# Optimization experiments

Hardware: AMD Instinct MI355X
Metric: run time of the kernel (lower is better)

The kernel has to match this reference:

```python
import jax, jax.numpy as jnp
import numpy as np

LN_EPS = 1e-5

def _ln(x, g, b):
    mu = jnp.mean(x, axis=-1, keepdims=True)
    var = jnp.mean((x - mu) ** 2, axis=-1, keepdims=True)
    return (x - mu) * jax.lax.rsqrt(var + LN_EPS) * g + b

def _gelu(x):
    return jax.nn.gelu(x, approximate=False)

def _time_embed(t, dim):
    # standard sinusoidal embedding on scalar times t: (B,) -> (B, dim)
    half = dim // 2
    freqs = jnp.exp(-jnp.log(10000.0) * jnp.arange(half, dtype=jnp.float32) / max(half - 1, 1))
    ang = t[:, None] * freqs[None, :]
    return jnp.concatenate([jnp.sin(ang), jnp.cos(ang)], axis=-1)

def setup_inputs() -> dict:
    key = jax.random.key(0)
    B, D, C, H, M = 1024, 128, 256, 512, 64
    ks = jax.random.split(key, 24)
    w = lambda k, shp: jax.random.normal(k, shp, dtype=jnp.float32) * 0.02
    inp = {
        "noise": jax.random.normal(ks[0], (B, D), dtype=jnp.float32),
        "context": jax.random.normal(ks[1], (B, C), dtype=jnp.float32),
        "support_memory": jax.random.normal(ks[2], (B, M, D), dtype=jnp.float32),
        "num_steps": 4,
        # memory adapter: LayerNorm(D) + Linear(D->H)
        "mem_ln_g": jnp.ones((D,), jnp.float32), "mem_ln_b": jnp.zeros((D,), jnp.float32),
        "Wa": w(ks[3], (D, H)), "ba": jnp.zeros((H,), jnp.float32),
        # attention projections H->H
        "Wq": w(ks[4], (H, H)), "bq": jnp.zeros((H,), jnp.float32),
        "Wk": w(ks[5], (H, H)), "bk": jnp.zeros((H,), jnp.float32),
        "Wv": w(ks[6], (H, H)), "bv": jnp.zeros((H,), jnp.float32),
        "Wo": w(ks[7], (H, H)), "bo": jnp.zeros((H,), jnp.float32),
        # particle proj: LN(D) + Linear(D->H) + GELU + Linear(H->H)
        "pp_ln_g": jnp.ones((D,), jnp.float32), "pp_ln_b": jnp.zeros((D,), jnp.float32),
        "Wp1": w(ks[8], (D, H)), "bp1": jnp.zeros((H,), jnp.float32),
        "Wp2": w(ks[9], (H, H)), "bp2": jnp.zeros((H,), jnp.float32),
        # context proj C->H
        "Wc": w(ks[10], (C, H)), "bc": jnp.zeros((H,), jnp.float32),
        # time proj H->H (on sinusoidal embedding of dim H)
        "Wt": w(ks[11], (H, H)), "bt": jnp.zeros((H,), jnp.float32),
        # fusion head: LN(4H) + Linear(4H->H) + GELU + Linear(H->D)
        "f_ln_g": jnp.ones((4 * H,), jnp.float32), "f_ln_b": jnp.zeros((4 * H,), jnp.float32),
        "Wf1": w(ks[12], (4 * H, H)), "bf1": jnp.zeros((H,), jnp.float32),
        "Wf2": w(ks[13], (H, D)), "bf2": jnp.zeros((D,), jnp.float32),
    }
    return inp

def reference(noise, context, support_memory, num_steps,
              mem_ln_g, mem_ln_b, Wa, ba,
              Wq, bq, Wk, bk, Wv, bv, Wo, bo,
              pp_ln_g, pp_ln_b, Wp1, bp1, Wp2, bp2,
              Wc, bc, Wt, bt,
              f_ln_g, f_ln_b, Wf1, bf1, Wf2, bf2):
    B, D = noise.shape
    H = Wq.shape[0]
    heads = 4
    dh = H // heads
    scale = dh ** -0.5

    # encode support memory once (solver-invariant), like encode_memory()
    enc = _ln(support_memory, mem_ln_g, mem_ln_b) @ Wa + ba            # (B, M, H)
    M = enc.shape[1]
    k_mem = (enc @ Wk + bk).reshape(B, M, heads, dh)                    # (B, M, h, dh)
    v_mem = (enc @ Wv + bv).reshape(B, M, heads, dh)
    ctx_h = context @ Wc + bc                                           # (B, H)

    def velocity(y, t):
        te = _time_embed(t, H) @ Wt + bt                                # (B, H)
        h = _gelu(_ln(y, pp_ln_g, pp_ln_b) @ Wp1 + bp1) @ Wp2 + bp2      # (B, H)
        q = (h @ Wq + bq).reshape(B, heads, dh)
        logits = jnp.einsum('bhd,bmhd->bhm', q, k_mem) * scale
        attn = jax.nn.softmax(logits, axis=-1)
        summ = jnp.einsum('bhm,bmhd->bhd', attn, v_mem).reshape(B, H)
        m = summ @ Wo + bo                                              # (B, H)
        z = jnp.concatenate([h, m, ctx_h, te], axis=-1)                 # (B, 4H)
        return _gelu(_ln(z, f_ln_g, f_ln_b) @ Wf1 + bf1) @ Wf2 + bf2     # (B, D)

    dt = 1.0 / float(num_steps)
    t0s = jnp.arange(num_steps, dtype=jnp.float32) * dt

    def heun_step(y, t0):
        tb0 = jnp.full((B,), t0, dtype=y.dtype)
        k1 = velocity(y, tb0)
        k2 = velocity(y + dt * k1, tb0 + dt)
        return y + 0.5 * dt * (k1 + k2), None

    y_final, _ = jax.lax.scan(heun_step, noise, t0s)
    return y_final
```

## Files before the change

kernel.cpp:

```cpp
#include <hip/hip_runtime.h>
#include <hip/hip_bf16.h>
#include <cstdint>
#include <cstddef>

#define LN_EPS 1e-5f

typedef __attribute__((ext_vector_type(8))) short short8;
typedef __attribute__((ext_vector_type(4))) float f32x4;

__device__ __forceinline__ float gelu_exact(float x) {
  return 0.5f * x * (1.0f + erff(x * 0.70710678118654752440f));
}
__device__ __forceinline__ float bflo(unsigned int x) {
  union { unsigned int i; float f; } v; v.i = x << 16; return v.f;
}
__device__ __forceinline__ float bfhi(unsigned int x) {
  union { unsigned int i; float f; } v; v.i = x & 0xffff0000u; return v.f;
}
__device__ __forceinline__ float bf2f(short s) {
  union { unsigned int i; float f; } v; v.i = ((unsigned int)(unsigned short)s) << 16; return v.f;
}
__device__ __forceinline__ short bf16s(float f) {
  __hip_bfloat16 h = __float2bfloat16(f);
  return *reinterpret_cast<short*>(&h);
}

__global__ __launch_bounds__(256) void ln_bf16_k(const float* __restrict__ X,
                                                 const float* __restrict__ KIN, float a,
                                                 const float* __restrict__ g,
                                                 const float* __restrict__ bb,
                                                 __hip_bfloat16* __restrict__ out, int rows) {
  int row = blockIdx.x * 4 + (threadIdx.x >> 6);
  if (row >= rows) return;
  int l = threadIdx.x & 63;
  size_t base = (size_t)row * 128;
  float x0 = X[base + l], x1 = X[base + l + 64];
  if (KIN) { x0 += a * KIN[base + l]; x1 += a * KIN[base + l + 64]; }
  float s = x0 + x1;
#pragma unroll
  for (int o = 32; o > 0; o >>= 1) s += __shfl_xor(s, o);
  float mu = s * (1.0f / 128.0f);
  float d0 = x0 - mu, d1 = x1 - mu;
  float v = d0 * d0 + d1 * d1;
#pragma unroll
  for (int o = 32; o > 0; o >>= 1) v += __shfl_xor(v, o);
  float rstd = rsqrtf(v * (1.0f / 128.0f) + LN_EPS);
  out[base + l] = __float2bfloat16(d0 * rstd * g[l] + bb[l]);
  out[base + l + 64] = __float2bfloat16(d1 * rstd * g[l + 64] + bb[l + 64]);
}

template <int BN, bool GELU_OUT, bool OUT_BF16>
__global__ __launch_bounds__(256) void gemm_mfma_k(
    const short* __restrict__ A, const short* __restrict__ WT,
    const float* __restrict__ bias, void* __restrict__ Cout,
    int K, int lda, int ldw, int ldc, float alpha,
    int hsA, int hsB, long hsC) {
  constexpr int NFRAG = BN / 16;
  constexpr int NB = (BN / 32) < 1 ? 1 : (BN / 32);
  __shared__ __align__(16) short As[2][64][72];
  __shared__ __align__(16) short Bs[2][BN][72];
  A += (size_t)blockIdx.z * hsA;
  WT += (size_t)blockIdx.z * hsB;
  const size_t cOff = (size_t)blockIdx.z * (size_t)hsC;
  const int tid = threadIdx.x;
  const int w = tid >> 6, l = tid & 63;
  const int row0 = blockIdx.y * 64, col0 = blockIdx.x * BN;
  f32x4 acc[NFRAG];
#pragma unroll
  for (int i = 0; i < NFRAG; ++i) acc[i] = (f32x4){0.f, 0.f, 0.f, 0.f};

  const int nt = K >> 6;
  short8 aR0, aR1;
  short8 bR[NB];
  auto loadA = [&](int t) {
    int k0 = t * 64;
    int c1 = tid + 256;
    aR0 = *(const short8*)(A + (size_t)(row0 + (tid >> 3)) * lda + k0 + (tid & 7) * 8);
    aR1 = *(const short8*)(A + (size_t)(row0 + (c1 >> 3)) * lda + k0 + (c1 & 7) * 8);
  };
  auto loadB = [&](int t) {
    int k0 = t * 64;
#pragma unroll
    for (int i = 0; i < NB; ++i) {
      int c = tid + i * 256;
      bR[i] = *(const short8*)(WT + (size_t)(col0 + (c >> 3)) * ldw + k0 + (c & 7) * 8);
    }
  };
  auto storeT = [&](int buf) {
    int c1 = tid + 256;
    *(short8*)&As[buf][tid >> 3][(tid & 7) * 8] = aR0;
    *(short8*)&As[buf][c1 >> 3][(c1 & 7) * 8] = aR1;
#pragma unroll
    for (int i = 0; i < NB; ++i) {
      int c = tid + i * 256;
      *(short8*)&Bs[buf][c >> 3][(c & 7) * 8] = bR[i];
    }
  };

  loadA(0);
  loadB(0);
  for (int t = 0; t < nt; ++t) {
    int buf = t & 1;
    storeT(buf);
    __syncthreads();
    if (t + 1 < nt) { loadA(t + 1); loadB(t + 1); }
    short8 af0 = *(const short8*)&As[buf][w * 16 + (l & 15)][(l >> 4) * 8];
    short8 af1 = *(const short8*)&As[buf][w * 16 + (l & 15)][(l >> 4) * 8 + 32];
#pragma unroll
    for (int nc = 0; nc < NFRAG; ++nc) {
      short8 bf0 = *(const short8*)&Bs[buf][nc * 16 + (l & 15)][(l >> 4) * 8];
      acc[nc] = __builtin_amdgcn_mfma_f32_16x16x32_bf16(af0, bf0, acc[nc], 0, 0, 0);
      short8 bf1 = *(const short8*)&Bs[buf][nc * 16 + (l & 15)][(l >> 4) * 8 + 32];
      acc[nc] = __builtin_amdgcn_mfma_f32_16x16x32_bf16(af1, bf1, acc[nc], 0, 0, 0);
    }
    __syncthreads();
  }
  const int cr = (l >> 4) * 4;
  const int cc = l & 15;
#pragma unroll
  for (int nc = 0; nc < NFRAG; ++nc) {
    int gc = col0 + nc * 16 + cc;
    float bv = bias ? bias[gc] : 0.0f;
#pragma unroll
    for (int r = 0; r < 4; ++r) {
      int gr = row0 + w * 16 + cr + r;
      float v = acc[nc][r] * alpha + bv;
      if (GELU_OUT) v = gelu_exact(v);
      if (OUT_BF16)
        ((__hip_bfloat16*)Cout)[cOff + (size_t)gr * ldc + gc] = __float2bfloat16(v);
      else
        ((float*)Cout)[cOff + (size_t)gr * ldc + gc] = v;
    }
  }
}

__global__ __launch_bounds__(256) void gemm_heun_k(
    const short* __restrict__ A, const short* __restrict__ WT,
    const float* __restrict__ bias, const float* __restrict__ yin,
    const float* __restrict__ kaux, float c0, float* __restrict__ outY) {
  __shared__ __align__(16) short As[2][64][72];
  __shared__ __align__(16) short Bs[2][32][72];
  const int tid = threadIdx.x;
  const int w = tid >> 6, l = tid & 63;
  const int row0 = blockIdx.y * 64, col0 = blockIdx.x * 32;
  f32x4 acc[2];
  acc[0] = (f32x4){0.f, 0.f, 0.f, 0.f};
  acc[1] = (f32x4){0.f, 0.f, 0.f, 0.f};
  short8 aR0, aR1, bR;
  auto loadA = [&](int t) {
    int k0 = t * 64;
    int c1 = tid + 256;
    aR0 = *(const short8*)(A + (size_t)(row0 + (tid >> 3)) * 512 + k0 + (tid & 7) * 8);
    aR1 = *(const short8*)(A + (size_t)(row0 + (c1 >> 3)) * 512 + k0 + (c1 & 7) * 8);
  };
  auto loadB = [&](int t) {
    int k0 = t * 64;
    bR = *(const short8*)(WT + (size_t)(col0 + (tid >> 3)) * 512 + k0 + (tid & 7) * 8);
  };
  auto storeT = [&](int buf) {
    int c1 = tid + 256;
    *(short8*)&As[buf][tid >> 3][(tid & 7) * 8] = aR0;
    *(short8*)&As[buf][c1 >> 3][(c1 & 7) * 8] = aR1;
    *(short8*)&Bs[buf][tid >> 3][(tid & 7) * 8] = bR;
  };
  loadA(0);
  loadB(0);
  for (int t = 0; t < 8; ++t) {
    int buf = t & 1;
    storeT(buf);
    __syncthreads();
    if (t + 1 < 8) { loadA(t + 1); loadB(t + 1); }
    short8 af0 = *(const short8*)&As[buf][w * 16 + (l & 15)][(l >> 4) * 8];
    short8 af1 = *(const short8*)&As[buf][w * 16 + (l & 15)][(l >> 4) * 8 + 32];
#pragma unroll
    for (int nc = 0; nc < 2; ++nc) {
      short8 bf0 = *(const short8*)&Bs[buf][nc * 16 + (l & 15)][(l >> 4) * 8];
      acc[nc] = __builtin_amdgcn_mfma_f32_16x16x32_bf16(af0, bf0, acc[nc], 0, 0, 0);
      short8 bf1 = *(const short8*)&Bs[buf][nc * 16 + (l & 15)][(l >> 4) * 8 + 32];
      acc[nc] = __builtin_amdgcn_mfma_f32_16x16x32_bf16(af1, bf1, acc[nc], 0, 0, 0);
    }
    __syncthreads();
  }
  const int cr = (l >> 4) * 4, cc = l & 15;
#pragma unroll
  for (int nc = 0; nc < 2; ++nc) {
    int gc = col0 + nc * 16 + cc;
    float bv = bias[gc];
#pragma unroll
    for (int r = 0; r < 4; ++r) {
      int gr = row0 + w * 16 + cr + r;
      float v = acc[nc][r] + bv;
      size_t idx = (size_t)gr * 128 + gc;
      outY[idx] = yin[idx] + c0 * (kaux[idx] + v);
    }
  }
}

struct TCBatch { const float* src[5]; short* dst[5]; };
__global__ __launch_bounds__(256) void transpose_cast_batch_k(TCBatch p) {
  const float* W = p.src[blockIdx.z];
  short* WT = p.dst[blockIdx.z];
  __shared__ float tile[64][65];
  int n0 = blockIdx.x * 64, k0 = blockIdx.y * 64;
#pragma unroll
  for (int i = 0; i < 16; ++i) {
    int e = threadIdx.x + i * 256;
    int r = e >> 6, c = e & 63;
    tile[r][c] = W[(size_t)(k0 + r) * 512 + n0 + c];
  }
  __syncthreads();
#pragma unroll
  for (int i = 0; i < 16; ++i) {
    int e = threadIdx.x + i * 256;
    int r = e >> 6, c = e & 63;
    WT[(size_t)(n0 + r) * 512 + k0 + c] = bf16s(tile[c][r]);
  }
}

__global__ __launch_bounds__(256) void transpose_cast_k(const float* __restrict__ W,
                                                        short* __restrict__ WT,
                                                        int K, int N) {
  __shared__ float tile[64][65];
  int n0 = blockIdx.x * 64, k0 = blockIdx.y * 64;
#pragma unroll
  for (int i = 0; i < 16; ++i) {
    int e = threadIdx.x + i * 256;
    int r = e >> 6, c = e & 63;
    tile[r][c] = W[(size_t)(k0 + r) * N + n0 + c];
  }
  __syncthreads();
#pragma unroll
  for (int i = 0; i < 16; ++i) {
    int e = threadIdx.x + i * 256;
    int r = e >> 6, c = e & 63;
    WT[(size_t)(n0 + r) * K + k0 + c] = bf16s(tile[c][r]);
  }
}

__global__ void cast_bf16_k(const float* __restrict__ src, short* __restrict__ dst, int n) {
  int i = blockIdx.x * blockDim.x + threadIdx.x;
  if (i < n) dst[i] = bf16s(src[i]);
}

__global__ __launch_bounds__(256) void bias_fuse_k(const float* __restrict__ va,
                                                   const float* __restrict__ Wx,
                                                   const float* __restrict__ bx,
                                                   float* __restrict__ out) {
  const int tid = threadIdx.x;
  const int j = blockIdx.x * 32 + (tid >> 3);
  const int kl = tid & 7;
  float s = 0.f;
  for (int k = kl; k < 512; k += 8) s += va[k] * Wx[(size_t)k * 512 + j];
  s += __shfl_xor(s, 1);
  s += __shfl_xor(s, 2);
  s += __shfl_xor(s, 4);
  if (kl == 0) out[j] = s + bx[j];
}

__global__ __launch_bounds__(256) void bqp_k(const float* __restrict__ bhqq,
                                             const short* __restrict__ Wak_bf,
                                             float scale, float* __restrict__ bqp) {
  const int tid = threadIdx.x;
  const int j = blockIdx.x * 32 + (tid >> 3);
  const int h = j >> 7, e = j & 127;
  const int kl = tid & 7;
  float s = 0.f;
  for (int d = kl; d < 128; d += 8)
    s += bhqq[h * 128 + d] * bf2f(Wak_bf[(size_t)e * 512 + h * 128 + d]);
  s += __shfl_xor(s, 1);
  s += __shfl_xor(s, 2);
  s += __shfl_xor(s, 4);
  if (kl == 0) bqp[j] = s * scale;
}

__global__ __launch_bounds__(512) void te_k(const float* __restrict__ Wt,
                                            const float* __restrict__ bt,
                                            float* __restrict__ te) {
  __shared__ float emb[512];
  const int ci = blockIdx.x;
  const float t = 0.25f * (float)((ci >> 1) + (ci & 1));
  const int j = threadIdx.x;
  if (j < 256) {
    float fr = expf(-9.210340371976184f * (float)j * (1.0f / 255.0f));
    float ang = t * fr;
    emb[j] = sinf(ang);
    emb[j + 256] = cosf(ang);
  }
  __syncthreads();
  float s0 = 0.f, s1 = 0.f, s2 = 0.f, s3 = 0.f;
  for (int k = 0; k < 512; k += 4) {
    s0 += emb[k] * Wt[(size_t)k * 512 + j];
    s1 += emb[k + 1] * Wt[(size_t)(k + 1) * 512 + j];
    s2 += emb[k + 2] * Wt[(size_t)(k + 2) * 512 + j];
    s3 += emb[k + 3] * Wt[(size_t)(k + 3) * 512 + j];
  }
  te[(size_t)ci * 512 + j] = bt[j] + ((s0 + s1) + (s2 + s3));
}

__global__ __launch_bounds__(256) void attn_k(const __hip_bfloat16* __restrict__ hq,
                                              const short* __restrict__ lnsm,
                                              __hip_bfloat16* __restrict__ sctx) {
  const int b = blockIdx.x;
  const int tid = threadIdx.x;
  const int w = tid >> 6, l = tid & 63;
  __shared__ __align__(16) short smt[64 * 128];
  __shared__ float qs[512];
  __shared__ float att[4][64];
  {
    unsigned int u = ((const unsigned int*)(hq + (size_t)b * 1024 + 512))[tid];
    qs[2 * tid] = bflo(u);
    qs[2 * tid + 1] = bfhi(u);
  }
  {
    const int m = tid >> 2;
    const short* src = lnsm + ((size_t)b * 64 + m) * 128;
#pragma unroll
    for (int j = 0; j < 4; ++j) {
      int c = (tid & 3) + 4 * j;
      short8 v = *(const short8*)(src + c * 8);
      *(short8*)&smt[m * 128 + ((c ^ (m & 7)) * 8)] = v;
    }
  }
  __syncthreads();
  const float* qh = qs + w * 128;
  float acc = 0.f;
#pragma unroll
  for (int i = 0; i < 16; ++i) {
    uint4 u = *(const uint4*)&smt[l * 128 + ((i ^ (l & 7)) * 8)];
    const int d = i * 8;
    acc += bflo(u.x) * qh[d + 0] + bfhi(u.x) * qh[d + 1] +
           bflo(u.y) * qh[d + 2] + bfhi(u.y) * qh[d + 3] +
           bflo(u.z) * qh[d + 4] + bfhi(u.z) * qh[d + 5] +
           bflo(u.w) * qh[d + 6] + bfhi(u.w) * qh[d + 7];
  }
  float mx = acc;
#pragma unroll
  for (int o = 32; o > 0; o >>= 1) mx = fmaxf(mx, __shfl_xor(mx, o));
  float e = expf(acc - mx);
  float se = e;
#pragma unroll
  for (int o = 32; o > 0; o >>= 1) se += __shfl_xor(se, o);
  att[w][l] = e / se;
  const int cb = l >> 2, doff = 2 * (l & 3);
  float a0 = 0.f, a1 = 0.f;
#pragma unroll 8
  for (int m = 0; m < 64; ++m) {
    float am = att[w][m];
    unsigned int u = *(const unsigned int*)&smt[m * 128 + ((cb ^ (m & 7)) * 8) + doff];
    a0 += am * bflo(u);
    a1 += am * bfhi(u);
  }
  unsigned int pr = ((unsigned int)(unsigned short)bf16s(a1) << 16) |
                    (unsigned int)(unsigned short)bf16s(a0);
  ((unsigned int*)(sctx + (size_t)b * 512 + w * 128))[l] = pr;
}

__global__ __launch_bounds__(512) void zln_k(const __hip_bfloat16* __restrict__ hq,
                                             const __hip_bfloat16* __restrict__ mo,
                                             const __hip_bfloat16* __restrict__ ctxh,
                                             const float* __restrict__ te_row,
                                             const float* __restrict__ g,
                                             const float* __restrict__ bb,
                                             __hip_bfloat16* __restrict__ zout) {
  const int b = blockIdx.x;
  const int tid = threadIdx.x;
  float v0 = __bfloat162float(hq[(size_t)b * 1024 + tid]);
  float v1 = __bfloat162float(mo[(size_t)b * 512 + tid]);
  float v2 = __bfloat162float(ctxh[(size_t)b * 512 + tid]);
  float v3 = te_row[tid];
  __shared__ float red[8];
  float s = v0 + v1 + v2 + v3;
#pragma unroll
  for (int o = 32; o > 0; o >>= 1) s += __shfl_xor(s, o);
  if ((tid & 63) == 0) red[tid >> 6] = s;
  __syncthreads();
  s = red[0] + red[1] + red[2] + red[3] + red[4] + red[5] + red[6] + red[7];
  float mu = s * (1.0f / 2048.0f);
  float d0 = v0 - mu, d1 = v1 - mu, d2 = v2 - mu, d3 = v3 - mu;
  float vv = d0 * d0 + d1 * d1 + d2 * d2 + d3 * d3;
  __syncthreads();
#pragma unroll
  for (int o = 32; o > 0; o >>= 1) vv += __shfl_xor(vv, o);
  if ((tid & 63) == 0) red[tid >> 6] = vv;
  __syncthreads();
  vv = red[0] + red[1] + red[2] + red[3] + red[4] + red[5] + red[6] + red[7];
  float rstd = rsqrtf(vv * (1.0f / 2048.0f) + LN_EPS);
  zout[(size_t)b * 2048 + tid] = __float2bfloat16(d0 * rstd * g[tid] + bb[tid]);
  zout[(size_t)b * 2048 + 512 + tid] = __float2bfloat16(d1 * rstd * g[512 + tid] + bb[512 + tid]);
  zout[(size_t)b * 2048 + 1024 + tid] = __float2bfloat16(d2 * rstd * g[1024 + tid] + bb[1024 + tid]);
  zout[(size_t)b * 2048 + 1536 + tid] = __float2bfloat16(d3 * rstd * g[1536 + tid] + bb[1536 + tid]);
}

extern "C" void kernel_launch(void* const* d_in, const int* in_sizes, int n_in,
                              void* d_out, int out_size, void* d_ws, size_t ws_size,
                              hipStream_t stream) {
  (void)in_sizes; (void)n_in; (void)out_size; (void)ws_size;
  const int B = 1024, Mm = 64;
  const int BMrows = B * Mm;
  const float ATTN_SCALE = 0.08838834764831845f;
  const size_t SL = (size_t)512 * 512;

  const float* noise = (const float*)d_in[0];
  const float* context = (const float*)d_in[1];
  const float* sm = (const float*)d_in[2];
  const float* mem_ln_g = (const float*)d_in[4];
  const float* mem_ln_b = (const float*)d_in[5];
  const float* Wa = (const float*)d_in[6];
  const float* ba = (const float*)d_in[7];
  const float* Wq = (const float*)d_in[8];
  const float* bq = (const float*)d_in[9];
  const float* Wk = (const float*)d_in[10];
  const float* bk = (const float*)d_in[11];
  (void)bk;
  const float* Wv = (const float*)d_in[12];
  const float* bv = (const float*)d_in[13];
  const float* Wo = (const float*)d_in[14];
  const float* bo = (const float*)d_in[15];
  const float* pp_ln_g = (const float*)d_in[16];
  const float* pp_ln_b = (const float*)d_in[17];
  const float* Wp1 = (const float*)d_in[18];
  const float* bp1 = (const float*)d_in[19];
  const float* Wp2 = (const float*)d_in[20];
  const float* bp2 = (const float*)d_in[21];
  const float* Wc = (const float*)d_in[22];
  const float* bc = (const float*)d_in[23];
  const float* Wt = (const float*)d_in[24];
  const float* bt = (const float*)d_in[25];
  const float* f_ln_g = (const float*)d_in[26];
  const float* f_ln_b = (const float*)d_in[27];
  const float* Wf1 = (const float*)d_in[28];
  const float* bf1 = (const float*)d_in[29];
  const float* Wf2 = (const float*)d_in[30];
  const float* bf2 = (const float*)d_in[31];
  float* out = (float*)d_out;

  char* wsb = (char*)d_ws;
  size_t off = 0;
  auto alloc = [&](size_t bytes) -> void* {
    off = (off + 255) & ~(size_t)255;
    void* p = wsb + off;
    off += bytes;
    return p;
  };
  short* lnsm = (short*)alloc((size_t)BMrows * 128 * 2);
  short* T512 = (short*)alloc(4 * SL * 2);
  short* WkT = T512;
  short* WvT = T512 + SL;
  short* WqT = T512 + 2 * SL;
  short* WoT = T512 + 3 * SL;
  short* Wp1T = (short*)alloc((size_t)512 * 128 * 2);
  short* WhqT = (short*)alloc((size_t)1024 * 512 * 2);
  short* WfoldT = (short*)alloc(SL * 2);
  short* WcT = (short*)alloc((size_t)512 * 256 * 2);
  short* Wf1T = (short*)alloc((size_t)512 * 2048 * 2);
  short* Wf2T = (short*)alloc((size_t)128 * 512 * 2);
  short* WaB = (short*)alloc((size_t)128 * 512 * 2);
  short* Wp2B = (short*)alloc(SL * 2);
  short* WakavB = (short*)alloc(2 * (size_t)128 * 512 * 2);
  short* Wak_bf = WakavB;
  short* Wav_bf = WakavB + (size_t)128 * 512;
  short* Wp2q_bf = (short*)alloc(SL * 2);
  float* bhq = (float*)alloc(1024 * 4);
  float* bofold = (float*)alloc(512 * 4);
  float* bhqq = (float*)alloc(512 * 4);
  float* bav = (float*)alloc(512 * 4);
  float* te_table = (float*)alloc(8 * 512 * 4);
  short* ctxh = (short*)alloc((size_t)B * 512 * 2);
  float* k1 = (float*)alloc((size_t)B * 128 * 4);
  float* ybuf = (float*)alloc((size_t)B * 128 * 4);
  short* ctxb = (short*)alloc((size_t)B * 256 * 2);
  short* yln = (short*)alloc((size_t)B * 128 * 2);
  short* hmid = (short*)alloc((size_t)B * 512 * 2);
  short* hqbuf = (short*)alloc((size_t)B * 1024 * 2);
  short* sctx = (short*)alloc((size_t)B * 512 * 2);
  short* mobuf = (short*)alloc((size_t)B * 512 * 2);
  short* zbuf = (short*)alloc((size_t)B * 2048 * 2);
  short* fmid = (short*)alloc((size_t)B * 512 * 2);

  ln_bf16_k<<<BMrows / 4, 256, 0, stream>>>(sm, nullptr, 0.f, mem_ln_g, mem_ln_b,
                                            (__hip_bfloat16*)lnsm, BMrows);
  cast_bf16_k<<<(128 * 512 + 255) / 256, 256, 0, stream>>>(Wa, WaB, 128 * 512);
  cast_bf16_k<<<(512 * 512 + 255) / 256, 256, 0, stream>>>(Wp2, Wp2B, 512 * 512);
  cast_bf16_k<<<(B * 256 + 255) / 256, 256, 0, stream>>>(context, ctxb, B * 256);
  {
    TCBatch p;
    p.src[0] = Wk; p.src[1] = Wv; p.src[2] = Wq; p.src[3] = Wo; p.src[4] = Wp2;
    p.dst[0] = WkT; p.dst[1] = WvT; p.dst[2] = WqT; p.dst[3] = WoT; p.dst[4] = WhqT;
    transpose_cast_batch_k<<<dim3(8, 8, 5), 256, 0, stream>>>(p);
  }
  transpose_cast_k<<<dim3(8, 2), 256, 0, stream>>>(Wp1, Wp1T, 128, 512);
  transpose_cast_k<<<dim3(8, 4), 256, 0, stream>>>(Wc, WcT, 256, 512);
  transpose_cast_k<<<dim3(8, 32), 256, 0, stream>>>(Wf1, Wf1T, 2048, 512);
  transpose_cast_k<<<dim3(2, 8), 256, 0, stream>>>(Wf2, Wf2T, 512, 128);
  gemm_mfma_k<64, false, true><<<dim3(8, 2, 2), 256, 0, stream>>>(
      WaB, WkT, nullptr, WakavB, 512, 512, 512, 512, 1.f, 0, (int)SL, 128 * 512);
  gemm_mfma_k<64, false, true><<<dim3(8, 8), 256, 0, stream>>>(
      Wp2B, WqT, nullptr, Wp2q_bf, 512, 512, 512, 512, 1.f, 0, 0, 0);
  gemm_mfma_k<64, false, true><<<dim3(8, 2, 4), 256, 0, stream>>>(
      Wak_bf, Wp2q_bf, nullptr, WhqT + SL, 128, 512, 512, 512, ATTN_SCALE,
      128, 128, 128 * 512);
  gemm_mfma_k<64, false, true><<<dim3(2, 8, 4), 256, 0, stream>>>(
      WoT, Wav_bf, nullptr, WfoldT, 128, 512, 512, 512, 1.f, 128, 128, 128);
  bias_fuse_k<<<16, 256, 0, stream>>>(bp2, Wq, bq, bhqq);
  bqp_k<<<16, 256, 0, stream>>>(bhqq, Wak_bf, ATTN_SCALE, bhq + 512);
  hipMemcpyAsync(bhq, bp2, 512 * 4, hipMemcpyDeviceToDevice, stream);
  bias_fuse_k<<<16, 256, 0, stream>>>(ba, Wv, bv, bav);
  bias_fuse_k<<<16, 256, 0, stream>>>(bav, Wo, bo, bofold);
  gemm_mfma_k<64, false, true><<<dim3(8, 16), 256, 0, stream>>>(
      ctxb, WcT, bc, ctxh, 256, 256, 256, 512, 1.f, 0, 0, 0);
  te_k<<<8, 512, 0, stream>>>(Wt, bt, te_table);

  const float dt = 0.25f;
  auto chain = [&](const float* ycur, const float* kin, float a, int tidx) {
    ln_bf16_k<<<B / 4, 256, 0, stream>>>(ycur, kin, a, pp_ln_g, pp_ln_b,
                                         (__hip_bfloat16*)yln, B);
    gemm_mfma_k<32, true, true><<<dim3(16, 16), 256, 0, stream>>>(
        yln, Wp1T, bp1, hmid, 128, 128, 128, 512, 1.f, 0, 0, 0);
    gemm_mfma_k<64, false, true><<<dim3(16, 16), 256, 0, stream>>>(
        hmid, WhqT, bhq, hqbuf, 512, 512, 512, 1024, 1.f, 0, 0, 0);
    attn_k<<<B, 256, 0, stream>>>((const __hip_bfloat16*)hqbuf, lnsm,
                                  (__hip_bfloat16*)sctx);
    gemm_mfma_k<32, false, true><<<dim3(16, 16), 256, 0, stream>>>(
        sctx, WfoldT, bofold, mobuf, 512, 512, 512, 512, 1.f, 0, 0, 0);
    zln_k<<<B, 512, 0, stream>>>((const __hip_bfloat16*)hqbuf, (const __hip_bfloat16*)mobuf,
                                 (const __hip_bfloat16*)ctxh, te_table + (size_t)tidx * 512,
                                 f_ln_g, f_ln_b, (__hip_bfloat16*)zbuf);
    gemm_mfma_k<32, true, true><<<dim3(16, 16), 256, 0, stream>>>(
        zbuf, Wf1T, bf1, fmid, 2048, 2048, 2048, 512, 1.f, 0, 0, 0);
  };

  const float* ycur = noise;
  for (int s = 0; s < 4; ++s) {
    chain(ycur, nullptr, 0.f, 2 * s);
    gemm_mfma_k<32, false, false><<<dim3(4, 16), 256, 0, stream>>>(
        fmid, Wf2T, bf2, k1, 512, 512, 512, 128, 1.f, 0, 0, 0);
    chain(ycur, k1, dt, 2 * s + 1);
    float* ynext = (s == 3) ? out : ybuf;
    gemm_heun_k<<<dim3(4, 16), 256, 0, stream>>>(
        fmid, Wf2T, bf2, ycur, k1, 0.5f * dt, ynext);
    ycur = ybuf;
  }
}
```

Measured before the change: 596.9 us.

## Replace LDS-tiled GEMMs in the ODE loop with single-wave register-direct MFMA kernels

```diff
diff --git a/kernel.cpp b/kernel.cpp
--- a/kernel.cpp
+++ b/kernel.cpp
@@ -47,6 +47,56 @@
   float rstd = rsqrtf(v * (1.0f / 128.0f) + LN_EPS);
   out[base + l] = __float2bfloat16(d0 * rstd * g[l] + bb[l]);
   out[base + l + 64] = __float2bfloat16(d1 * rstd * g[l + 64] + bb[l + 64]);
+}
+
+template <int K, int COLS, int EPI, bool GELU_OUT, bool OUT_BF16>
+__global__ __launch_bounds__(64) void gemm_wave_k(
+    const short* __restrict__ A, const short* __restrict__ WT,
+    const float* __restrict__ bias, void* __restrict__ Cout,
+    int lda, int ldw, int ldc,
+    const float* __restrict__ yin, const float* __restrict__ kaux, float c0) {
+  constexpr int F = COLS / 16;
+  const int l = threadIdx.x;
+  const int row0 = blockIdx.y * 16, col0 = blockIdx.x * COLS;
+  const int rl = l & 15, k8 = (l >> 4) * 8;
+  const short* pA = A + (size_t)(row0 + rl) * lda + k8;
+  const short* pB[F];
+#pragma unroll
+  for (int f = 0; f < F; ++f)
+    pB[f] = WT + (size_t)(col0 + f * 16 + rl) * ldw + k8;
+  f32x4 acc[F];
+#pragma unroll
+  for (int f = 0; f < F; ++f) acc[f] = (f32x4){0.f, 0.f, 0.f, 0.f};
+#pragma unroll
+  for (int k0 = 0; k0 < K; k0 += 32) {
+    short8 a = *(const short8*)(pA + k0);
+    short8 b[F];
+#pragma unroll
+    for (int f = 0; f < F; ++f) b[f] = *(const short8*)(pB[f] + k0);
+#pragma unroll
+    for (int f = 0; f < F; ++f)
+      acc[f] = __builtin_amdgcn_mfma_f32_16x16x32_bf16(a, b[f], acc[f], 0, 0, 0);
+  }
+  const int cr = (l >> 4) * 4, cc = l & 15;
+#pragma unroll
+  for (int f = 0; f < F; ++f) {
+    int gc = col0 + f * 16 + cc;
+    float bv = bias ? bias[gc] : 0.0f;
+#pragma unroll
+    for (int r = 0; r < 4; ++r) {
+      int gr = row0 + cr + r;
+      float v = acc[f][r] + bv;
+      if (GELU_OUT) v = gelu_exact(v);
+      size_t idx = (size_t)gr * ldc + gc;
+      if (EPI == 2) {
+        ((float*)Cout)[idx] = yin[idx] + c0 * (kaux[idx] + v);
+      } else if (OUT_BF16) {
+        ((__hip_bfloat16*)Cout)[idx] = __float2bfloat16(v);
+      } else {
+        ((float*)Cout)[idx] = v;
+      }
+    }
+  }
 }
 
 template <int BN, bool GELU_OUT, bool OUT_BF16>
@@ -130,68 +180,6 @@
         ((__hip_bfloat16*)Cout)[cOff + (size_t)gr * ldc + gc] = __float2bfloat16(v);
       else
         ((float*)Cout)[cOff + (size_t)gr * ldc + gc] = v;
-    }
-  }
-}
-
-__global__ __launch_bounds__(256) void gemm_heun_k(
-    const short* __restrict__ A, const short* __restrict__ WT,
-    const float* __restrict__ bias, const float* __restrict__ yin,
-    const float* __restrict__ kaux, float c0, float* __restrict__ outY) {
-  __shared__ __align__(16) short As[2][64][72];
-  __shared__ __align__(16) short Bs[2][32][72];
-  const int tid = threadIdx.x;
-  const int w = tid >> 6, l = tid & 63;
-  const int row0 = blockIdx.y * 64, col0 = blockIdx.x * 32;
-  f32x4 acc[2];
-  acc[0] = (f32x4){0.f, 0.f, 0.f, 0.f};
-  acc[1] = (f32x4){0.f, 0.f, 0.f, 0.f};
-  short8 aR0, aR1, bR;
-  auto loadA = [&](int t) {
-    int k0 = t * 64;
-    int c1 = tid + 256;
-    aR0 = *(const short8*)(A + (size_t)(row0 + (tid >> 3)) * 512 + k0 + (tid & 7) * 8);
-    aR1 = *(const short8*)(A + (size_t)(row0 + (c1 >> 3)) * 512 + k0 + (c1 & 7) * 8);
-  };
-  auto loadB = [&](int t) {
-    int k0 = t * 64;
-    bR = *(const short8*)(WT + (size_t)(col0 + (tid >> 3)) * 512 + k0 + (tid & 7) * 8);
-  };
-  auto storeT = [&](int buf) {
-    int c1 = tid + 256;
-    *(short8*)&As[buf][tid >> 3][(tid & 7) * 8] = aR0;
-    *(short8*)&As[buf][c1 >> 3][(c1 & 7) * 8] = aR1;
-    *(short8*)&Bs[buf][tid >> 3][(tid & 7) * 8] = bR;
-  };
-  loadA(0);
-  loadB(0);
-  for (int t = 0; t < 8; ++t) {
-    int buf = t & 1;
-    storeT(buf);
-    __syncthreads();
-    if (t + 1 < 8) { loadA(t + 1); loadB(t + 1); }
-    short8 af0 = *(const short8*)&As[buf][w * 16 + (l & 15)][(l >> 4) * 8];
-    short8 af1 = *(const short8*)&As[buf][w * 16 + (l & 15)][(l >> 4) * 8 + 32];
-#pragma unroll
-    for (int nc = 0; nc < 2; ++nc) {
-      short8 bf0 = *(const short8*)&Bs[buf][nc * 16 + (l & 15)][(l >> 4) * 8];
-      acc[nc] = __builtin_amdgcn_mfma_f32_16x16x32_bf16(af0, bf0, acc[nc], 0, 0, 0);
-      short8 bf1 = *(const short8*)&Bs[buf][nc * 16 + (l & 15)][(l >> 4) * 8 + 32];
-      acc[nc] = __builtin_amdgcn_mfma_f32_16x16x32_bf16(af1, bf1, acc[nc], 0, 0, 0);
-    }
-    __syncthreads();
-  }
-  const int cr = (l >> 4) * 4, cc = l & 15;
-#pragma unroll
-  for (int nc = 0; nc < 2; ++nc) {
-    int gc = col0 + nc * 16 + cc;
-    float bv = bias[gc];
-#pragma unroll
-    for (int r = 0; r < 4; ++r) {
-      int gr = row0 + w * 16 + cr + r;
-      float v = acc[nc][r] + bv;
-      size_t idx = (size_t)gr * 128 + gc;
-      outY[idx] = yin[idx] + c0 * (kaux[idx] + v);
     }
   }
 }
@@ -514,30 +502,30 @@
   auto chain = [&](const float* ycur, const float* kin, float a, int tidx) {
     ln_bf16_k<<<B / 4, 256, 0, stream>>>(ycur, kin, a, pp_ln_g, pp_ln_b,
                                          (__hip_bfloat16*)yln, B);
-    gemm_mfma_k<32, true, true><<<dim3(16, 16), 256, 0, stream>>>(
-        yln, Wp1T, bp1, hmid, 128, 128, 128, 512, 1.f, 0, 0, 0);
-    gemm_mfma_k<64, false, true><<<dim3(16, 16), 256, 0, stream>>>(
-        hmid, WhqT, bhq, hqbuf, 512, 512, 512, 1024, 1.f, 0, 0, 0);
+    gemm_wave_k<128, 64, 0, true, true><<<dim3(8, 64), 64, 0, stream>>>(
+        yln, Wp1T, bp1, hmid, 128, 128, 512, nullptr, nullptr, 0.f);
+    gemm_wave_k<512, 64, 0, false, true><<<dim3(16, 64), 64, 0, stream>>>(
+        hmid, WhqT, bhq, hqbuf, 512, 512, 1024, nullptr, nullptr, 0.f);
     attn_k<<<B, 256, 0, stream>>>((const __hip_bfloat16*)hqbuf, lnsm,
                                   (__hip_bfloat16*)sctx);
-    gemm_mfma_k<32, false, true><<<dim3(16, 16), 256, 0, stream>>>(
-        sctx, WfoldT, bofold, mobuf, 512, 512, 512, 512, 1.f, 0, 0, 0);
+    gemm_wave_k<512, 64, 0, false, true><<<dim3(8, 64), 64, 0, stream>>>(
+        sctx, WfoldT, bofold, mobuf, 512, 512, 512, nullptr, nullptr, 0.f);
     zln_k<<<B, 512, 0, stream>>>((const __hip_bfloat16*)hqbuf, (const __hip_bfloat16*)mobuf,
                                  (const __hip_bfloat16*)ctxh, te_table + (size_t)tidx * 512,
                                  f_ln_g, f_ln_b, (__hip_bfloat16*)zbuf);
-    gemm_mfma_k<32, true, true><<<dim3(16, 16), 256, 0, stream>>>(
-        zbuf, Wf1T, bf1, fmid, 2048, 2048, 2048, 512, 1.f, 0, 0, 0);
+    gemm_wave_k<2048, 64, 0, true, true><<<dim3(8, 64), 64, 0, stream>>>(
+        zbuf, Wf1T, bf1, fmid, 2048, 2048, 512, nullptr, nullptr, 0.f);
   };
 
   const float* ycur = noise;
   for (int s = 0; s < 4; ++s) {
     chain(ycur, nullptr, 0.f, 2 * s);
-    gemm_mfma_k<32, false, false><<<dim3(4, 16), 256, 0, stream>>>(
-        fmid, Wf2T, bf2, k1, 512, 512, 512, 128, 1.f, 0, 0, 0);
+    gemm_wave_k<512, 32, 0, false, false><<<dim3(4, 64), 64, 0, stream>>>(
+        fmid, Wf2T, bf2, k1, 512, 512, 128, nullptr, nullptr, 0.f);
     chain(ycur, k1, dt, 2 * s + 1);
     float* ynext = (s == 3) ? out : ybuf;
-    gemm_heun_k<<<dim3(4, 16), 256, 0, stream>>>(
-        fmid, Wf2T, bf2, ycur, k1, 0.5f * dt, ynext);
+    gemm_wave_k<512, 32, 2, false, false><<<dim3(4, 64), 64, 0, stream>>>(
+        fmid, Wf2T, bf2, ynext, 512, 512, 128, ycur, k1, 0.5f * dt);
     ycur = ybuf;
   }
 }
```

New measurement: 662.3 us. 11.0% more time.
